# Kernel tuning notes

Measured on AMD Instinct MI355X. Metric: run time of the kernel, lower is better.

The kernel has to match this reference:

```python
import jax, jax.numpy as jnp
import numpy as np

N, E, FEAT, H, C = 50000, 800000, 256, 256, 64
THETA = 0.5


def _l2norm(x, eps=1e-12):
    n = jnp.sqrt(jnp.sum(x * x, axis=-1, keepdims=True))
    return x / jnp.maximum(n, eps)


def _gcn_conv(x, row, col, W, b):
    # x: [N, Fin]; row/col: [E+N] (self loops already appended); all edge weights are 1
    n = x.shape[0]
    h = x @ W                                                   # [N, Fout]
    ones = jnp.ones(row.shape, dtype=h.dtype)
    deg = jax.ops.segment_sum(ones, row, num_segments=n)        # in-degree over rows
    deg_safe = jnp.where(deg > 0, deg, 1.0)
    dinv = jnp.where(deg > 0, jax.lax.rsqrt(deg_safe), 0.0)
    norm = dinv[row] * dinv[col]                                # [E+N]
    msg = norm[:, None] * h[col]                                # gather + weight
    out = jax.ops.segment_sum(msg, row, num_segments=n)         # scatter-add
    return out + b


def setup_inputs() -> dict:
    key = jax.random.key(0)
    ks = jax.random.split(key, 10)
    edge_index = jax.random.randint(ks[0], (2, E), 0, N, dtype=jnp.int32)
    neg_edge_index = jax.random.randint(ks[1], (2, E), 0, N, dtype=jnp.int32)
    features = jax.random.normal(ks[2], (N, FEAT), dtype=jnp.float32)
    label_smoothing = jax.random.uniform(ks[3], (E,), dtype=jnp.float32)
    W1 = jax.random.normal(ks[4], (FEAT, H), dtype=jnp.float32) / np.sqrt(FEAT)
    b1 = jnp.zeros((H,), dtype=jnp.float32)
    W2 = jax.random.normal(ks[5], (H, H), dtype=jnp.float32) / np.sqrt(H)
    b2 = jnp.zeros((H,), dtype=jnp.float32)
    Wy = jax.random.normal(ks[6], (H, C), dtype=jnp.float32) / np.sqrt(H)
    by = jnp.zeros((C,), dtype=jnp.float32)
    return {"edge_index": edge_index, "features": features,
            "label_smoothing": label_smoothing, "neg_edge_index": neg_edge_index,
            "W1": W1, "b1": b1, "W2": W2, "b2": b2, "Wy": Wy, "by": by}


def reference(edge_index, features, label_smoothing, neg_edge_index,
              W1, b1, W2, b2, Wy, by):
    n = features.shape[0]
    self_idx = jnp.arange(n, dtype=edge_index.dtype)
    row = jnp.concatenate([edge_index[0], self_idx])
    col = jnp.concatenate([edge_index[1], self_idx])

    # GCN (dropout=0.0)
    x1 = jax.nn.relu(_gcn_conv(features, row, col, W1, b1))
    x2 = _gcn_conv(x1, row, col, W2, b2)
    rep = _l2norm(x2)
    rep = _l2norm(rep)  # second normalize in q_phi1.forward
    y = rep @ Wy + by

    # reconstruct_loss (i<j filtering done via static-shape masks)
    e0, e1 = edge_index[0], edge_index[1]
    n0, n1 = neg_edge_index[0], neg_edge_index[1]
    pos_mask = (e0 < e1).astype(rep.dtype)
    neg_mask = (n0 < n1).astype(rep.dtype)

    neg_w = jax.nn.relu(jnp.sum(rep[n0] * rep[n1], axis=1))
    pos_w = jax.nn.relu(jnp.sum(rep[e0] * rep[e1], axis=1))
    pos_fsim = jnp.sum(features[e0] * features[e1], axis=1)
    pos = pos_fsim * THETA + pos_w * (1.0 - THETA)

    n_pos = jnp.sum(pos_mask)
    n_neg = jnp.sum(neg_mask)
    neg_loss = jnp.sum(neg_mask * neg_w * neg_w)
    pos_loss = jnp.sum(pos_mask * (pos - label_smoothing) ** 2)
    rec_loss = (neg_loss + pos_loss) * n / (n_neg + n_pos)
    return rep, rec_loss, y
```

## Files before the change

### kernel.cpp

```cpp
#include <hip/hip_runtime.h>
#include <hip/hip_bf16.h>

#define FEAT 256
#define HDIM 256
#define CDIM 64
#define THETA 0.5f
#define APAD 264

typedef float floatx2 __attribute__((ext_vector_type(2)));
typedef __attribute__((ext_vector_type(8))) short bf16x8;
typedef __attribute__((ext_vector_type(4))) float f32x4;

__device__ __forceinline__ unsigned short f2bf(float f) {
    unsigned int u = __float_as_uint(f);
    u += 0x7fffu + ((u >> 16) & 1u);
    return (unsigned short)(u >> 16);
}
__device__ __forceinline__ unsigned char f2f8(float f) {
    int w = __builtin_amdgcn_cvt_pk_fp8_f32(f, f, 0, false);
    return (unsigned char)(w & 0xff);
}

__global__ __launch_bounds__(256) void prep(const int* __restrict__ e0, const int* __restrict__ e1,
                                            const int* __restrict__ n0, const int* __restrict__ n1,
                                            int* deg, int* __restrict__ blkP, int* __restrict__ blkN,
                                            const float* __restrict__ features, unsigned char* __restrict__ feat8,
                                            const float* __restrict__ W1, unsigned short* __restrict__ Wt1,
                                            const float* __restrict__ W2, unsigned short* __restrict__ Wt2,
                                            const float* __restrict__ Wy, unsigned short* __restrict__ WyT,
                                            int E, int n8, int ebk, int f8bk) {
    const int b = blockIdx.x;
    const int tid = threadIdx.x;
    if (b < ebk) {
        const int i = b * 256 + tid;
        const int lane = tid & 63;
        const int w = tid >> 6;
        bool vp = false, vn = false;
        if (i < E) {
            int a = e0[i], bb = e1[i];
            atomicAdd(&deg[a], 1);
            vp = a < bb;
            vn = n0[i] < n1[i];
        }
        unsigned long long mp = __ballot(vp);
        unsigned long long mn = __ballot(vn);
        __shared__ int s[8];
        if (lane == 0) {
            s[w] = __popcll(mp);
            s[4 + w] = __popcll(mn);
        }
        __syncthreads();
        if (tid == 0) blkP[b] = s[0] + s[1] + s[2] + s[3];
        if (tid == 1) blkN[b] = s[4] + s[5] + s[6] + s[7];
    } else if (b < ebk + f8bk) {
        int i = (b - ebk) * 256 + tid;
        if (i < n8) {
            float4 a = ((const float4*)features)[2 * i];
            float4 v = ((const float4*)features)[2 * i + 1];
            int w0 = __builtin_amdgcn_cvt_pk_fp8_f32(a.x, a.y, 0, false);
            w0 = __builtin_amdgcn_cvt_pk_fp8_f32(a.z, a.w, w0, true);
            int w1 = __builtin_amdgcn_cvt_pk_fp8_f32(v.x, v.y, 0, false);
            w1 = __builtin_amdgcn_cvt_pk_fp8_f32(v.z, v.w, w1, true);
            uint2 o;
            o.x = (unsigned int)w0;
            o.y = (unsigned int)w1;
            ((uint2*)feat8)[i] = o;
        }
    } else if (b < ebk + f8bk + 256) {
        int k = b - ebk - f8bk;
        Wt1[(size_t)tid * 256 + k] = f2bf(W1[(size_t)k * 256 + tid]);
    } else if (b < ebk + f8bk + 512) {
        int k = b - ebk - f8bk - 256;
        Wt2[(size_t)tid * 256 + k] = f2bf(W2[(size_t)k * 256 + tid]);
    } else {
        int b3 = b - ebk - f8bk - 512;
        int n = tid & 63;
        int k = b3 * 4 + (tid >> 6);
        WyT[(size_t)n * 256 + k] = f2bf(Wy[(size_t)k * 64 + n]);
    }
}

__global__ __launch_bounds__(256) void scan1_dinv(const int* __restrict__ deg,
                                                  int* __restrict__ rowptr,
                                                  int* __restrict__ blkS,
                                                  float* __restrict__ dinv, int N) {
    __shared__ int sh[256];
    const int tid = threadIdx.x;
    const int i = blockIdx.x * 256 + tid;
    int v = (i < N) ? deg[i] : 0;
    if (i < N) dinv[i] = rsqrtf((float)(v + 1));
    sh[tid] = v;
    __syncthreads();
#pragma unroll
    for (int off = 1; off < 256; off <<= 1) {
        int t = (tid >= off) ? sh[tid - off] : 0;
        __syncthreads();
        sh[tid] += t;
        __syncthreads();
    }
    if (i < N) rowptr[i] = sh[tid] - v;
    if (tid == 255) blkS[blockIdx.x] = sh[255];
}

__global__ __launch_bounds__(256) void scan2x(int* __restrict__ blkS, int nbn,
                                              int* __restrict__ blkP, int* __restrict__ blkN,
                                              int* __restrict__ cnt, int nb) {
    const int tid = threadIdx.x;
    if (blockIdx.x == 0) {
        __shared__ int part[256];
        const int chunk = (nbn + 255) / 256;
        const int s = tid * chunk;
        const int e = min(s + chunk, nbn);
        int sum = 0;
        for (int i = s; i < e; ++i) sum += blkS[i];
        part[tid] = sum;
        __syncthreads();
#pragma unroll
        for (int off = 1; off < 256; off <<= 1) {
            int t = (tid >= off) ? part[tid - off] : 0;
            __syncthreads();
            part[tid] += t;
            __syncthreads();
        }
        int run = part[tid] - sum;
        for (int i = s; i < e; ++i) {
            int v = blkS[i];
            blkS[i] = run;
            run += v;
        }
    } else {
        __shared__ int partP[256], partN[256];
        const int chunk = (nb + 255) / 256;
        const int s = tid * chunk;
        const int e = min(s + chunk, nb);
        int sp = 0, sn = 0;
        for (int i = s; i < e; ++i) { sp += blkP[i]; sn += blkN[i]; }
        partP[tid] = sp;
        partN[tid] = sn;
        __syncthreads();
#pragma unroll
        for (int off = 1; off < 256; off <<= 1) {
            int tp = (tid >= off) ? partP[tid - off] : 0;
            int tn = (tid >= off) ? partN[tid - off] : 0;
            __syncthreads();
            partP[tid] += tp;
            partN[tid] += tn;
            __syncthreads();
        }
        int runP = partP[tid] - sp;
        int runN = partN[tid] - sn;
        for (int i = s; i < e; ++i) {
            int vp = blkP[i], vn = blkN[i];
            blkP[i] = runP;
            blkN[i] = runN;
            runP += vp;
            runN += vn;
        }
        if (tid == 255) { cnt[0] = runP; cnt[1] = runN; }
    }
}

__global__ __launch_bounds__(256) void scan3_scatter(int* __restrict__ rowptr, int* __restrict__ cursor,
                                                     const int* __restrict__ blkS, int N, int E, int nbn,
                                                     const int* __restrict__ e0, const int* __restrict__ e1,
                                                     const int* __restrict__ n0, const int* __restrict__ n1,
                                                     const float* __restrict__ ls,
                                                     const int* __restrict__ blkP, const int* __restrict__ blkN,
                                                     int2* __restrict__ posAB, float* __restrict__ posLS,
                                                     int2* __restrict__ negCD) {
    const int b = blockIdx.x;
    const int tid = threadIdx.x;
    if (b < nbn) {
        const int i = b * 256 + tid;
        if (i < N) {
            int v = rowptr[i] + blkS[b];
            rowptr[i] = v;
            cursor[i] = v;
        }
        if (i == 0) rowptr[N] = E;
        return;
    }
    const int eb = b - nbn;
    const int i = eb * 256 + tid;
    const int lane = tid & 63;
    const int w = tid >> 6;
    const unsigned long long below = (lane == 0) ? 0ull : ((1ull << lane) - 1ull);
    int a = 0, bb = 0, c = 0, d = 0;
    float lsv = 0.f;
    bool vp = false, vn = false;
    if (i < E) {
        a = e0[i]; bb = e1[i];
        c = n0[i]; d = n1[i];
        vp = a < bb;
        vn = c < d;
        if (vp) lsv = ls[i];
    }
    unsigned long long mp = __ballot(vp);
    unsigned long long mn = __ballot(vn);
    __shared__ int sP[4], sN[4];
    if (lane == 0) {
        sP[w] = __popcll(mp);
        sN[w] = __popcll(mn);
    }
    __syncthreads();
    int baseP = blkP[eb];
    int baseN = blkN[eb];
    for (int q = 0; q < 4; ++q) {
        if (q < w) { baseP += sP[q]; baseN += sN[q]; }
    }
    if (vp) {
        int ofs = __popcll(mp & below);
        posAB[baseP + ofs] = make_int2(a, bb);
        posLS[baseP + ofs] = lsv;
    }
    if (vn) {
        int ofs = __popcll(mn & below);
        negCD[baseN + ofs] = make_int2(c, d);
    }
}

__global__ __launch_bounds__(256) void bucket_edges(const int* __restrict__ e0,
                                                    const int* __restrict__ e1,
                                                    int* cursor, int* __restrict__ colIdx, int E) {
    int i = blockIdx.x * 256 + threadIdx.x;
    if (i < E) {
        int r = e0[i];
        int pos = atomicAdd(&cursor[r], 1);
        colIdx[pos] = e1[i];
    }
}

__device__ __forceinline__ void gemm_core_f8out(const unsigned short* Al,
                                                const unsigned short* __restrict__ Wt,
                                                unsigned char* __restrict__ out,
                                                int m0, int wv, int lane, int M) {
    f32x4 acc[4][4] = {};
    const int r16 = lane & 15;
    const int kg8 = (lane >> 4) * 8;
    const unsigned short* wbase = Wt + ((size_t)(wv * 64 + r16)) * 256 + kg8;
    const unsigned short* abase = Al + r16 * APAD + kg8;

#pragma unroll
    for (int k0 = 0; k0 < 256; k0 += 32) {
        bf16x8 af[4], bfr[4];
#pragma unroll
        for (int mi = 0; mi < 4; ++mi)
            af[mi] = *(const bf16x8*)&abase[mi * 16 * APAD + k0];
#pragma unroll
        for (int ni = 0; ni < 4; ++ni)
            bfr[ni] = *(const bf16x8*)&wbase[ni * 16 * 256 + k0];
#pragma unroll
        for (int mi = 0; mi < 4; ++mi)
#pragma unroll
            for (int ni = 0; ni < 4; ++ni)
                acc[mi][ni] = __builtin_amdgcn_mfma_f32_16x16x32_bf16(af[mi], bfr[ni], acc[mi][ni], 0, 0, 0);
    }

#pragma unroll
    for (int mi = 0; mi < 4; ++mi) {
        int rbase = m0 + mi * 16 + ((lane >> 4) << 2);
#pragma unroll
        for (int ni = 0; ni < 4; ++ni) {
            int col = (wv << 6) + (ni << 4) + (lane & 15);
#pragma unroll
            for (int j = 0; j < 4; ++j) {
                int row = rbase + j;
                if (row < M) out[(size_t)row * 256 + col] = f2f8(acc[mi][ni][j]);
            }
        }
    }
}

__global__ __launch_bounds__(256) void gemm_mfma_f32A(const float* __restrict__ A,
                                                      const unsigned short* __restrict__ Wt,
                                                      unsigned char* __restrict__ out, int M) {
    __shared__ unsigned short Al[64 * APAD];
    const int tid = threadIdx.x;
    const int m0 = blockIdx.x * 64;
#pragma unroll
    for (int i = 0; i < 8; ++i) {
        int u = i * 256 + tid;
        int r = u >> 5;
        int c8 = (u & 31) * 8;
        int row = m0 + r;
        float4 v0, v1;
        if (row < M) {
            v0 = *(const float4*)&A[(size_t)row * 256 + c8];
            v1 = *(const float4*)&A[(size_t)row * 256 + c8 + 4];
        } else {
            v0 = make_float4(0.f, 0.f, 0.f, 0.f);
            v1 = v0;
        }
        uint4 o;
        o.x = (unsigned int)f2bf(v0.x) | ((unsigned int)f2bf(v0.y) << 16);
        o.y = (unsigned int)f2bf(v0.z) | ((unsigned int)f2bf(v0.w) << 16);
        o.z = (unsigned int)f2bf(v1.x) | ((unsigned int)f2bf(v1.y) << 16);
        o.w = (unsigned int)f2bf(v1.z) | ((unsigned int)f2bf(v1.w) << 16);
        *(uint4*)&Al[r * APAD + c8] = o;
    }
    __syncthreads();
    gemm_core_f8out(Al, Wt, out, m0, tid >> 6, tid & 63, M);
}

__global__ __launch_bounds__(256) void gemm_mfma_b16A(const unsigned short* __restrict__ A,
                                                      const unsigned short* __restrict__ Wt,
                                                      unsigned char* __restrict__ out, int M) {
    __shared__ unsigned short Al[64 * APAD];
    const int tid = threadIdx.x;
    const int m0 = blockIdx.x * 64;
#pragma unroll
    for (int i = 0; i < 8; ++i) {
        int u = i * 256 + tid;
        int r = u >> 5;
        int c8 = (u & 31) * 8;
        int row = m0 + r;
        uint4 o = make_uint4(0, 0, 0, 0);
        if (row < M) o = *(const uint4*)&A[(size_t)row * 256 + c8];
        *(uint4*)&Al[r * APAD + c8] = o;
    }
    __syncthreads();
    gemm_core_f8out(Al, Wt, out, m0, tid >> 6, tid & 63, M);
}

__global__ __launch_bounds__(256) void gemm_wy_f8A(const unsigned char* __restrict__ rep8,
                                                   const unsigned short* __restrict__ WyT,
                                                   const float* __restrict__ bias,
                                                   float* __restrict__ out, int M) {
    __shared__ unsigned short Al[64 * APAD];
    const int tid = threadIdx.x;
    const int m0 = blockIdx.x * 64;
    const int wv = tid >> 6;
    const int lane = tid & 63;

#pragma unroll
    for (int i = 0; i < 4; ++i) {
        int u = i * 256 + tid;
        int r = u >> 4;
        int c16 = (u & 15) * 16;
        int row = m0 + r;
        uint4 v = make_uint4(0, 0, 0, 0);
        if (row < M) v = *(const uint4*)&rep8[(size_t)row * 256 + c16];
        unsigned int ws[4] = {v.x, v.y, v.z, v.w};
        unsigned int ow[8];
#pragma unroll
        for (int q = 0; q < 4; ++q) {
            floatx2 lo = __builtin_amdgcn_cvt_pk_f32_fp8((int)ws[q], false);
            floatx2 hi = __builtin_amdgcn_cvt_pk_f32_fp8((int)ws[q], true);
            ow[2 * q] = (unsigned int)f2bf(lo.x) | ((unsigned int)f2bf(lo.y) << 16);
            ow[2 * q + 1] = (unsigned int)f2bf(hi.x) | ((unsigned int)f2bf(hi.y) << 16);
        }
        *(uint4*)&Al[r * APAD + c16] = make_uint4(ow[0], ow[1], ow[2], ow[3]);
        *(uint4*)&Al[r * APAD + c16 + 8] = make_uint4(ow[4], ow[5], ow[6], ow[7]);
    }
    __syncthreads();

    f32x4 acc[4] = {};
    const int r16 = lane & 15;
    const int kg8 = (lane >> 4) * 8;
    const unsigned short* wbase = WyT + ((size_t)(wv * 16 + r16)) * 256 + kg8;
    const unsigned short* abase = Al + r16 * APAD + kg8;

#pragma unroll
    for (int k0 = 0; k0 < 256; k0 += 32) {
        bf16x8 bfr = *(const bf16x8*)&wbase[k0];
#pragma unroll
        for (int mi = 0; mi < 4; ++mi) {
            bf16x8 af = *(const bf16x8*)&abase[mi * 16 * APAD + k0];
            acc[mi] = __builtin_amdgcn_mfma_f32_16x16x32_bf16(af, bfr, acc[mi], 0, 0, 0);
        }
    }

    int col = (wv << 4) + (lane & 15);
    float bv = bias[col];
#pragma unroll
    for (int mi = 0; mi < 4; ++mi) {
        int rbase = m0 + mi * 16 + ((lane >> 4) << 2);
#pragma unroll
        for (int j = 0; j < 4; ++j) {
            int row = rbase + j;
            if (row < M) out[(size_t)row * 64 + col] = acc[mi][j] + bv;
        }
    }
}

template <int DO_NORM>
__global__ __launch_bounds__(256) void spmm_gather_f8(const int* __restrict__ rowptr,
                                                      const int* __restrict__ colIdx,
                                                      const unsigned char* __restrict__ h8,
                                                      const float* __restrict__ dinv,
                                                      const float* __restrict__ bias,
                                                      unsigned short* __restrict__ out_b16,
                                                      float* __restrict__ rep,
                                                      unsigned char* __restrict__ rep8,
                                                      int N) {
    int row = (blockIdx.x * 256 + threadIdx.x) >> 5;
    int l = threadIdx.x & 31;
    if (row >= N) return;
    int beg = rowptr[row];
    int end = rowptr[row + 1];
    float a0 = 0.f, a1 = 0.f, a2 = 0.f, a3 = 0.f, a4 = 0.f, a5 = 0.f, a6 = 0.f, a7 = 0.f;
    int j = beg;
    for (; j + 3 < end; j += 4) {
        int cc[4];
#pragma unroll
        for (int q = 0; q < 4; ++q) cc[q] = colIdx[j + q];
        float ww[4];
#pragma unroll
        for (int q = 0; q < 4; ++q) ww[q] = dinv[cc[q]];
        uint2 uu[4];
#pragma unroll
        for (int q = 0; q < 4; ++q) uu[q] = *(const uint2*)&h8[(size_t)cc[q] * 256 + l * 8];
#pragma unroll
        for (int q = 0; q < 4; ++q) {
            floatx2 p0 = __builtin_amdgcn_cvt_pk_f32_fp8((int)uu[q].x, false);
            floatx2 p1 = __builtin_amdgcn_cvt_pk_f32_fp8((int)uu[q].x, true);
            floatx2 p2 = __builtin_amdgcn_cvt_pk_f32_fp8((int)uu[q].y, false);
            floatx2 p3 = __builtin_amdgcn_cvt_pk_f32_fp8((int)uu[q].y, true);
            a0 = fmaf(ww[q], p0.x, a0); a1 = fmaf(ww[q], p0.y, a1);
            a2 = fmaf(ww[q], p1.x, a2); a3 = fmaf(ww[q], p1.y, a3);
            a4 = fmaf(ww[q], p2.x, a4); a5 = fmaf(ww[q], p2.y, a5);
            a6 = fmaf(ww[q], p3.x, a6); a7 = fmaf(ww[q], p3.y, a7);
        }
    }
    for (; j < end; ++j) {
        int c = colIdx[j];
        float w = dinv[c];
        uint2 u = *(const uint2*)&h8[(size_t)c * 256 + l * 8];
        floatx2 p0 = __builtin_amdgcn_cvt_pk_f32_fp8((int)u.x, false);
        floatx2 p1 = __builtin_amdgcn_cvt_pk_f32_fp8((int)u.x, true);
        floatx2 p2 = __builtin_amdgcn_cvt_pk_f32_fp8((int)u.y, false);
        floatx2 p3 = __builtin_amdgcn_cvt_pk_f32_fp8((int)u.y, true);
        a0 = fmaf(w, p0.x, a0); a1 = fmaf(w, p0.y, a1);
        a2 = fmaf(w, p1.x, a2); a3 = fmaf(w, p1.y, a3);
        a4 = fmaf(w, p2.x, a4); a5 = fmaf(w, p2.y, a5);
        a6 = fmaf(w, p3.x, a6); a7 = fmaf(w, p3.y, a7);
    }
    float di = dinv[row];
    float s = di * di;
    uint2 us = *(const uint2*)&h8[(size_t)row * 256 + l * 8];
    floatx2 s0 = __builtin_amdgcn_cvt_pk_f32_fp8((int)us.x, false);
    floatx2 s1 = __builtin_amdgcn_cvt_pk_f32_fp8((int)us.x, true);
    floatx2 s2 = __builtin_amdgcn_cvt_pk_f32_fp8((int)us.y, false);
    floatx2 s3 = __builtin_amdgcn_cvt_pk_f32_fp8((int)us.y, true);
    float4 bv0 = *(const float4*)&bias[l * 8];
    float4 bv1 = *(const float4*)&bias[l * 8 + 4];
    float r0 = fmaf(di, a0, fmaf(s, s0.x, bv0.x));
    float r1 = fmaf(di, a1, fmaf(s, s0.y, bv0.y));
    float r2 = fmaf(di, a2, fmaf(s, s1.x, bv0.z));
    float r3 = fmaf(di, a3, fmaf(s, s1.y, bv0.w));
    float r4 = fmaf(di, a4, fmaf(s, s2.x, bv1.x));
    float r5 = fmaf(di, a5, fmaf(s, s2.y, bv1.y));
    float r6 = fmaf(di, a6, fmaf(s, s3.x, bv1.z));
    float r7 = fmaf(di, a7, fmaf(s, s3.y, bv1.w));
    if (DO_NORM == 0) {
        r0 = fmaxf(r0, 0.f); r1 = fmaxf(r1, 0.f); r2 = fmaxf(r2, 0.f); r3 = fmaxf(r3, 0.f);
        r4 = fmaxf(r4, 0.f); r5 = fmaxf(r5, 0.f); r6 = fmaxf(r6, 0.f); r7 = fmaxf(r7, 0.f);
        uint4 o;
        o.x = (unsigned int)f2bf(r0) | ((unsigned int)f2bf(r1) << 16);
        o.y = (unsigned int)f2bf(r2) | ((unsigned int)f2bf(r3) << 16);
        o.z = (unsigned int)f2bf(r4) | ((unsigned int)f2bf(r5) << 16);
        o.w = (unsigned int)f2bf(r6) | ((unsigned int)f2bf(r7) << 16);
        *(uint4*)&out_b16[(size_t)row * 256 + l * 8] = o;
    } else {
        float ss = r0 * r0 + r1 * r1 + r2 * r2 + r3 * r3 + r4 * r4 + r5 * r5 + r6 * r6 + r7 * r7;
#pragma unroll
        for (int o = 1; o < 32; o <<= 1) ss += __shfl_xor(ss, o);
        float inv = 1.0f / fmaxf(sqrtf(ss), 1e-12f);
        r0 *= inv; r1 *= inv; r2 *= inv; r3 *= inv;
        r4 *= inv; r5 *= inv; r6 *= inv; r7 *= inv;
        float ss2 = r0 * r0 + r1 * r1 + r2 * r2 + r3 * r3 + r4 * r4 + r5 * r5 + r6 * r6 + r7 * r7;
#pragma unroll
        for (int o = 1; o < 32; o <<= 1) ss2 += __shfl_xor(ss2, o);
        float inv2 = 1.0f / fmaxf(sqrtf(ss2), 1e-12f);
        r0 *= inv2; r1 *= inv2; r2 *= inv2; r3 *= inv2;
        r4 *= inv2; r5 *= inv2; r6 *= inv2; r7 *= inv2;
        *(float4*)&rep[(size_t)row * 256 + l * 8] = make_float4(r0, r1, r2, r3);
        *(float4*)&rep[(size_t)row * 256 + l * 8 + 4] = make_float4(r4, r5, r6, r7);
        int w0 = __builtin_amdgcn_cvt_pk_fp8_f32(r0, r1, 0, false);
        w0 = __builtin_amdgcn_cvt_pk_fp8_f32(r2, r3, w0, true);
        int w1 = __builtin_amdgcn_cvt_pk_fp8_f32(r4, r5, 0, false);
        w1 = __builtin_amdgcn_cvt_pk_fp8_f32(r6, r7, w1, true);
        uint2 o;
        o.x = (unsigned int)w0;
        o.y = (unsigned int)w1;
        *(uint2*)&rep8[(size_t)row * 256 + l * 8] = o;
    }
}

__device__ __forceinline__ float dot16fp8(uint4 x, uint4 y) {
    float s = 0.f;
    const unsigned int xs[4] = {x.x, x.y, x.z, x.w};
    const unsigned int ys[4] = {y.x, y.y, y.z, y.w};
#pragma unroll
    for (int i = 0; i < 4; ++i) {
        floatx2 xl = __builtin_amdgcn_cvt_pk_f32_fp8((int)xs[i], false);
        floatx2 xh = __builtin_amdgcn_cvt_pk_f32_fp8((int)xs[i], true);
        floatx2 yl = __builtin_amdgcn_cvt_pk_f32_fp8((int)ys[i], false);
        floatx2 yh = __builtin_amdgcn_cvt_pk_f32_fp8((int)ys[i], true);
        s += xl.x * yl.x + xl.y * yl.y + xh.x * yh.x + xh.y * yh.y;
    }
    return s;
}

__global__ __launch_bounds__(256) void loss_all(const int2* __restrict__ posAB,
                                                const float* __restrict__ posLS,
                                                const int2* __restrict__ negCD,
                                                const int* __restrict__ cnt,
                                                const unsigned char* __restrict__ rep8,
                                                const unsigned char* __restrict__ feat8,
                                                float* accum) {
    const int tid = threadIdx.x;
    const int l8 = tid & 7;
    const int grp = (blockIdx.x * 256 + tid) >> 3;
    const int ngrp = gridDim.x * 32;
    const int P = cnt[0];
    const int T = P + cnt[1];
    float ap = 0.f, an = 0.f;
    for (int g = grp; g < T; g += ngrp) {
        if (g < P) {
            int2 ab = posAB[g];
            const uint4* pra = (const uint4*)&rep8[(size_t)ab.x * 256 + l8 * 32];
            const uint4* prb = (const uint4*)&rep8[(size_t)ab.y * 256 + l8 * 32];
            const uint4* pfa = (const uint4*)&feat8[(size_t)ab.x * 256 + l8 * 32];
            const uint4* pfb = (const uint4*)&feat8[(size_t)ab.y * 256 + l8 * 32];
            uint4 ra0 = pra[0], ra1 = pra[1];
            uint4 rb0 = prb[0], rb1 = prb[1];
            uint4 fa0 = pfa[0], fa1 = pfa[1];
            uint4 fb0 = pfb[0], fb1 = pfb[1];
            float dp = dot16fp8(ra0, rb0) + dot16fp8(ra1, rb1);
            float df = dot16fp8(fa0, fb0) + dot16fp8(fa1, fb1);
#pragma unroll
            for (int o = 1; o < 8; o <<= 1) {
                dp += __shfl_xor(dp, o);
                df += __shfl_xor(df, o);
            }
            if (l8 == 0) {
                float pw = fmaxf(dp, 0.f);
                float pos = THETA * df + (1.0f - THETA) * pw;
                float t = pos - posLS[g];
                ap += t * t;
            }
        } else {
            int2 cd = negCD[g - P];
            const uint4* prc = (const uint4*)&rep8[(size_t)cd.x * 256 + l8 * 32];
            const uint4* prd = (const uint4*)&rep8[(size_t)cd.y * 256 + l8 * 32];
            uint4 rc0 = prc[0], rc1 = prc[1];
            uint4 rd0 = prd[0], rd1 = prd[1];
            float dn = dot16fp8(rc0, rd0) + dot16fp8(rc1, rd1);
#pragma unroll
            for (int o = 1; o < 8; o <<= 1) dn += __shfl_xor(dn, o);
            if (l8 == 0) {
                float nwt = fmaxf(dn, 0.f);
                an += nwt * nwt;
            }
        }
    }
#pragma unroll
    for (int o = 1; o < 64; o <<= 1) {
        ap += __shfl_xor(ap, o);
        an += __shfl_xor(an, o);
    }
    __shared__ float s[4][2];
    if ((tid & 63) == 0) {
        s[tid >> 6][0] = ap;
        s[tid >> 6][1] = an;
    }
    __syncthreads();
    if (tid == 0) {
        unsafeAtomicAdd(&accum[0], s[0][0] + s[1][0] + s[2][0] + s[3][0]);
        unsafeAtomicAdd(&accum[1], s[0][1] + s[1][1] + s[2][1] + s[3][1]);
    }
}

__global__ void loss_final(const float* __restrict__ accum, const int* __restrict__ cnt,
                           float* __restrict__ out, int N) {
    out[0] = (accum[0] + accum[1]) * (float)N / (float)(cnt[0] + cnt[1]);
}

extern "C" void kernel_launch(void* const* d_in, const int* in_sizes, int n_in,
                              void* d_out, int out_size, void* d_ws, size_t ws_size,
                              hipStream_t stream) {
    const int* edge = (const int*)d_in[0];
    const float* features = (const float*)d_in[1];
    const float* ls = (const float*)d_in[2];
    const int* nedge = (const int*)d_in[3];
    const float* W1 = (const float*)d_in[4];
    const float* b1 = (const float*)d_in[5];
    const float* W2 = (const float*)d_in[6];
    const float* b2 = (const float*)d_in[7];
    const float* Wy = (const float*)d_in[8];
    const float* by = (const float*)d_in[9];

    const int E = in_sizes[0] / 2;
    const int N = in_sizes[1] / FEAT;
    const int* e0 = edge;
    const int* e1 = edge + E;
    const int* n0 = nedge;
    const int* n1 = nedge + E;

    float* rep = (float*)d_out;
    float* rec = rep + (size_t)N * 256;
    float* y = rec + 1;

    char* base = (char*)d_ws;
    size_t off = 0;
    auto carve = [&](size_t bytes) -> void* {
        void* p = base + off;
        off += (bytes + 1023) & ~(size_t)1023;
        return p;
    };
    int* deg = (int*)carve((size_t)N * 4);
    float* dinv = (float*)carve((size_t)N * 4);
    float* accum = (float*)carve(16);
    int* cnt = (int*)carve(16);
    int* rowptr = (int*)carve((size_t)(N + 1) * 4);
    int* cursor = (int*)carve((size_t)N * 4);
    int* colIdx = (int*)carve((size_t)E * 4);
    unsigned char* h8 = (unsigned char*)carve((size_t)N * 256);
    unsigned short* x1B = (unsigned short*)carve((size_t)N * 256 * 2);
    unsigned char* feat8 = (unsigned char*)carve((size_t)N * 256);
    unsigned char* rep8 = (unsigned char*)carve((size_t)N * 256);
    unsigned short* Wt1 = (unsigned short*)carve(256 * 256 * 2);
    unsigned short* Wt2 = (unsigned short*)carve(256 * 256 * 2);
    unsigned short* WyT = (unsigned short*)carve(64 * 256 * 2);
    int2* posAB = (int2*)carve((size_t)E * 8);
    float* posLS = (float*)carve((size_t)E * 4);
    int2* negCD = (int2*)carve((size_t)E * 8);
    const int ebk = (E + 255) / 256;
    int* blkP = (int*)carve((size_t)ebk * 4);
    int* blkN = (int*)carve((size_t)ebk * 4);
    const int nbn = (N + 255) / 256;
    int* blkS = (int*)carve((size_t)nbn * 4);

    const int n8 = N * 256 / 8;
    const int f8bk = (n8 + 255) / 256;
    const int gblk = (N + 63) / 64;
    const int wblk32 = (N + 7) / 8;

    hipMemsetAsync(deg, 0, (size_t)N * 4, stream);
    hipMemsetAsync(accum, 0, 16, stream);

    prep<<<ebk + f8bk + 512 + 64, 256, 0, stream>>>(e0, e1, n0, n1, deg, blkP, blkN,
                                                    features, feat8, W1, Wt1, W2, Wt2, Wy, WyT,
                                                    E, n8, ebk, f8bk);

    scan1_dinv<<<nbn, 256, 0, stream>>>(deg, rowptr, blkS, dinv, N);
    scan2x<<<2, 256, 0, stream>>>(blkS, nbn, blkP, blkN, cnt, ebk);
    scan3_scatter<<<nbn + ebk, 256, 0, stream>>>(rowptr, cursor, blkS, N, E, nbn,
                                                 e0, e1, n0, n1, ls, blkP, blkN, posAB, posLS, negCD);
    bucket_edges<<<ebk, 256, 0, stream>>>(e0, e1, cursor, colIdx, E);

    gemm_mfma_f32A<<<gblk, 256, 0, stream>>>(features, Wt1, h8, N);
    spmm_gather_f8<0><<<wblk32, 256, 0, stream>>>(rowptr, colIdx, h8, dinv, b1, x1B, nullptr, nullptr, N);

    gemm_mfma_b16A<<<gblk, 256, 0, stream>>>(x1B, Wt2, h8, N);
    spmm_gather_f8<1><<<wblk32, 256, 0, stream>>>(rowptr, colIdx, h8, dinv, b2, nullptr, rep, rep8, N);

    gemm_wy_f8A<<<gblk, 256, 0, stream>>>(rep8, WyT, by, y, N);

    loss_all<<<2048, 256, 0, stream>>>(posAB, posLS, negCD, cnt, rep8, feat8, accum);
    loss_final<<<1, 1, 0, stream>>>(accum, cnt, rec, N);
}
```

Before: 370.8 us.

## Prescale GEMM output by dinv, fuse feature fp8 cast, interleave rep/feat rows

The GEMM epilogues now multiply each output row by dinv[row], so the SpMM gather no longer loads a per-neighbor dinv and just sums fp8 values. The fp8 cast of features moves out of the prep kernel into the first GEMM's A-load, removing a separate pass over the features array. rep8 and feat8 are interleaved into one 512-byte-per-node buffer so the positive-edge loss fetches both from adjacent memory. Scaling before fp8 quantization slightly changes rounding, and the wider row stride halves locality for negative-edge and Wy reads.

```diff
diff --git a/kernel.cpp b/kernel.cpp
--- a/kernel.cpp
+++ b/kernel.cpp
@@ -24,11 +24,10 @@
 __global__ __launch_bounds__(256) void prep(const int* __restrict__ e0, const int* __restrict__ e1,
                                             const int* __restrict__ n0, const int* __restrict__ n1,
                                             int* deg, int* __restrict__ blkP, int* __restrict__ blkN,
-                                            const float* __restrict__ features, unsigned char* __restrict__ feat8,
                                             const float* __restrict__ W1, unsigned short* __restrict__ Wt1,
                                             const float* __restrict__ W2, unsigned short* __restrict__ Wt2,
                                             const float* __restrict__ Wy, unsigned short* __restrict__ WyT,
-                                            int E, int n8, int ebk, int f8bk) {
+                                            int E, int ebk) {
     const int b = blockIdx.x;
     const int tid = threadIdx.x;
     if (b < ebk) {
@@ -52,28 +51,14 @@
         __syncthreads();
         if (tid == 0) blkP[b] = s[0] + s[1] + s[2] + s[3];
         if (tid == 1) blkN[b] = s[4] + s[5] + s[6] + s[7];
-    } else if (b < ebk + f8bk) {
-        int i = (b - ebk) * 256 + tid;
-        if (i < n8) {
-            float4 a = ((const float4*)features)[2 * i];
-            float4 v = ((const float4*)features)[2 * i + 1];
-            int w0 = __builtin_amdgcn_cvt_pk_fp8_f32(a.x, a.y, 0, false);
-            w0 = __builtin_amdgcn_cvt_pk_fp8_f32(a.z, a.w, w0, true);
-            int w1 = __builtin_amdgcn_cvt_pk_fp8_f32(v.x, v.y, 0, false);
-            w1 = __builtin_amdgcn_cvt_pk_fp8_f32(v.z, v.w, w1, true);
-            uint2 o;
-            o.x = (unsigned int)w0;
-            o.y = (unsigned int)w1;
-            ((uint2*)feat8)[i] = o;
-        }
-    } else if (b < ebk + f8bk + 256) {
-        int k = b - ebk - f8bk;
+    } else if (b < ebk + 256) {
+        int k = b - ebk;
         Wt1[(size_t)tid * 256 + k] = f2bf(W1[(size_t)k * 256 + tid]);
-    } else if (b < ebk + f8bk + 512) {
-        int k = b - ebk - f8bk - 256;
+    } else if (b < ebk + 512) {
+        int k = b - ebk - 256;
         Wt2[(size_t)tid * 256 + k] = f2bf(W2[(size_t)k * 256 + tid]);
     } else {
-        int b3 = b - ebk - f8bk - 512;
+        int b3 = b - ebk - 512;
         int n = tid & 63;
         int k = b3 * 4 + (tid >> 6);
         WyT[(size_t)n * 256 + k] = f2bf(Wy[(size_t)k * 64 + n]);
@@ -231,6 +216,7 @@
 }
 
 __device__ __forceinline__ void gemm_core_f8out(const unsigned short* Al,
+                                                const float* sd,
                                                 const unsigned short* __restrict__ Wt,
                                                 unsigned char* __restrict__ out,
                                                 int m0, int wv, int lane, int M) {
@@ -265,18 +251,22 @@
 #pragma unroll
             for (int j = 0; j < 4; ++j) {
                 int row = rbase + j;
-                if (row < M) out[(size_t)row * 256 + col] = f2f8(acc[mi][ni][j]);
+                if (row < M) out[(size_t)row * 256 + col] = f2f8(sd[row - m0] * acc[mi][ni][j]);
             }
         }
     }
 }
 
 __global__ __launch_bounds__(256) void gemm_mfma_f32A(const float* __restrict__ A,
+                                                      const float* __restrict__ dinv,
                                                       const unsigned short* __restrict__ Wt,
-                                                      unsigned char* __restrict__ out, int M) {
+                                                      unsigned char* __restrict__ out,
+                                                      unsigned char* __restrict__ repfeat8, int M) {
     __shared__ unsigned short Al[64 * APAD];
+    __shared__ float sd[64];
     const int tid = threadIdx.x;
     const int m0 = blockIdx.x * 64;
+    if (tid < 64) sd[tid] = (m0 + tid < M) ? dinv[m0 + tid] : 0.f;
 #pragma unroll
     for (int i = 0; i < 8; ++i) {
         int u = i * 256 + tid;
@@ -297,17 +287,30 @@
         o.z = (unsigned int)f2bf(v1.x) | ((unsigned int)f2bf(v1.y) << 16);
         o.w = (unsigned int)f2bf(v1.z) | ((unsigned int)f2bf(v1.w) << 16);
         *(uint4*)&Al[r * APAD + c8] = o;
+        if (row < M) {
+            int w0 = __builtin_amdgcn_cvt_pk_fp8_f32(v0.x, v0.y, 0, false);
+            w0 = __builtin_amdgcn_cvt_pk_fp8_f32(v0.z, v0.w, w0, true);
+            int w1 = __builtin_amdgcn_cvt_pk_fp8_f32(v1.x, v1.y, 0, false);
+            w1 = __builtin_amdgcn_cvt_pk_fp8_f32(v1.z, v1.w, w1, true);
+            uint2 f;
+            f.x = (unsigned int)w0;
+            f.y = (unsigned int)w1;
+            *(uint2*)&repfeat8[(size_t)row * 512 + 256 + c8] = f;
+        }
     }
     __syncthreads();
-    gemm_core_f8out(Al, Wt, out, m0, tid >> 6, tid & 63, M);
+    gemm_core_f8out(Al, sd, Wt, out, m0, tid >> 6, tid & 63, M);
 }
 
 __global__ __launch_bounds__(256) void gemm_mfma_b16A(const unsigned short* __restrict__ A,
+                                                      const float* __restrict__ dinv,
                                                       const unsigned short* __restrict__ Wt,
                                                       unsigned char* __restrict__ out, int M) {
     __shared__ unsigned short Al[64 * APAD];
+    __shared__ float sd[64];
     const int tid = threadIdx.x;
     const int m0 = blockIdx.x * 64;
+    if (tid < 64) sd[tid] = (m0 + tid < M) ? dinv[m0 + tid] : 0.f;
 #pragma unroll
     for (int i = 0; i < 8; ++i) {
         int u = i * 256 + tid;
@@ -319,10 +322,10 @@
         *(uint4*)&Al[r * APAD + c8] = o;
     }
     __syncthreads();
-    gemm_core_f8out(Al, Wt, out, m0, tid >> 6, tid & 63, M);
-}
-
-__global__ __launch_bounds__(256) void gemm_wy_f8A(const unsigned char* __restrict__ rep8,
+    gemm_core_f8out(Al, sd, Wt, out, m0, tid >> 6, tid & 63, M);
+}
+
+__global__ __launch_bounds__(256) void gemm_wy_f8A(const unsigned char* __restrict__ repfeat8,
                                                    const unsigned short* __restrict__ WyT,
                                                    const float* __restrict__ bias,
                                                    float* __restrict__ out, int M) {
@@ -339,7 +342,7 @@
         int c16 = (u & 15) * 16;
         int row = m0 + r;
         uint4 v = make_uint4(0, 0, 0, 0);
-        if (row < M) v = *(const uint4*)&rep8[(size_t)row * 256 + c16];
+        if (row < M) v = *(const uint4*)&repfeat8[(size_t)row * 512 + c16];
         unsigned int ws[4] = {v.x, v.y, v.z, v.w};
         unsigned int ow[8];
 #pragma unroll
@@ -386,12 +389,12 @@
 template <int DO_NORM>
 __global__ __launch_bounds__(256) void spmm_gather_f8(const int* __restrict__ rowptr,
                                                       const int* __restrict__ colIdx,
-                                                      const unsigned char* __restrict__ h8,
+                                                      const unsigned char* __restrict__ g8,
                                                       const float* __restrict__ dinv,
                                                       const float* __restrict__ bias,
                                                       unsigned short* __restrict__ out_b16,
                                                       float* __restrict__ rep,
-                                                      unsigned char* __restrict__ rep8,
+                                                      unsigned char* __restrict__ repfeat8,
                                                       int N) {
     int row = (blockIdx.x * 256 + threadIdx.x) >> 5;
     int l = threadIdx.x & 31;
@@ -404,54 +407,45 @@
         int cc[4];
 #pragma unroll
         for (int q = 0; q < 4; ++q) cc[q] = colIdx[j + q];
-        float ww[4];
-#pragma unroll
-        for (int q = 0; q < 4; ++q) ww[q] = dinv[cc[q]];
         uint2 uu[4];
 #pragma unroll
-        for (int q = 0; q < 4; ++q) uu[q] = *(const uint2*)&h8[(size_t)cc[q] * 256 + l * 8];
+        for (int q = 0; q < 4; ++q) uu[q] = *(const uint2*)&g8[(size_t)cc[q] * 256 + l * 8];
 #pragma unroll
         for (int q = 0; q < 4; ++q) {
             floatx2 p0 = __builtin_amdgcn_cvt_pk_f32_fp8((int)uu[q].x, false);
             floatx2 p1 = __builtin_amdgcn_cvt_pk_f32_fp8((int)uu[q].x, true);
             floatx2 p2 = __builtin_amdgcn_cvt_pk_f32_fp8((int)uu[q].y, false);
             floatx2 p3 = __builtin_amdgcn_cvt_pk_f32_fp8((int)uu[q].y, true);
-            a0 = fmaf(ww[q], p0.x, a0); a1 = fmaf(ww[q], p0.y, a1);
-            a2 = fmaf(ww[q], p1.x, a2); a3 = fmaf(ww[q], p1.y, a3);
-            a4 = fmaf(ww[q], p2.x, a4); a5 = fmaf(ww[q], p2.y, a5);
-            a6 = fmaf(ww[q], p3.x, a6); a7 = fmaf(ww[q], p3.y, a7);
+            a0 += p0.x; a1 += p0.y; a2 += p1.x; a3 += p1.y;
+            a4 += p2.x; a5 += p2.y; a6 += p3.x; a7 += p3.y;
         }
     }
     for (; j < end; ++j) {
         int c = colIdx[j];
-        float w = dinv[c];
-        uint2 u = *(const uint2*)&h8[(size_t)c * 256 + l * 8];
+        uint2 u = *(const uint2*)&g8[(size_t)c * 256 + l * 8];
         floatx2 p0 = __builtin_amdgcn_cvt_pk_f32_fp8((int)u.x, false);
         floatx2 p1 = __builtin_amdgcn_cvt_pk_f32_fp8((int)u.x, true);
         floatx2 p2 = __builtin_amdgcn_cvt_pk_f32_fp8((int)u.y, false);
         floatx2 p3 = __builtin_amdgcn_cvt_pk_f32_fp8((int)u.y, true);
-        a0 = fmaf(w, p0.x, a0); a1 = fmaf(w, p0.y, a1);
-        a2 = fmaf(w, p1.x, a2); a3 = fmaf(w, p1.y, a3);
-        a4 = fmaf(w, p2.x, a4); a5 = fmaf(w, p2.y, a5);
-        a6 = fmaf(w, p3.x, a6); a7 = fmaf(w, p3.y, a7);
+        a0 += p0.x; a1 += p0.y; a2 += p1.x; a3 += p1.y;
+        a4 += p2.x; a5 += p2.y; a6 += p3.x; a7 += p3.y;
     }
     float di = dinv[row];
-    float s = di * di;
-    uint2 us = *(const uint2*)&h8[(size_t)row * 256 + l * 8];
+    uint2 us = *(const uint2*)&g8[(size_t)row * 256 + l * 8];
     floatx2 s0 = __builtin_amdgcn_cvt_pk_f32_fp8((int)us.x, false);
     floatx2 s1 = __builtin_amdgcn_cvt_pk_f32_fp8((int)us.x, true);
     floatx2 s2 = __builtin_amdgcn_cvt_pk_f32_fp8((int)us.y, false);
     floatx2 s3 = __builtin_amdgcn_cvt_pk_f32_fp8((int)us.y, true);
     float4 bv0 = *(const float4*)&bias[l * 8];
     float4 bv1 = *(const float4*)&bias[l * 8 + 4];
-    float r0 = fmaf(di, a0, fmaf(s, s0.x, bv0.x));
-    float r1 = fmaf(di, a1, fmaf(s, s0.y, bv0.y));
-    float r2 = fmaf(di, a2, fmaf(s, s1.x, bv0.z));
-    float r3 = fmaf(di, a3, fmaf(s, s1.y, bv0.w));
-    float r4 = fmaf(di, a4, fmaf(s, s2.x, bv1.x));
-    float r5 = fmaf(di, a5, fmaf(s, s2.y, bv1.y));
-    float r6 = fmaf(di, a6, fmaf(s, s3.x, bv1.z));
-    float r7 = fmaf(di, a7, fmaf(s, s3.y, bv1.w));
+    float r0 = fmaf(di, a0 + s0.x, bv0.x);
+    float r1 = fmaf(di, a1 + s0.y, bv0.y);
+    float r2 = fmaf(di, a2 + s1.x, bv0.z);
+    float r3 = fmaf(di, a3 + s1.y, bv0.w);
+    float r4 = fmaf(di, a4 + s2.x, bv1.x);
+    float r5 = fmaf(di, a5 + s2.y, bv1.y);
+    float r6 = fmaf(di, a6 + s3.x, bv1.z);
+    float r7 = fmaf(di, a7 + s3.y, bv1.w);
     if (DO_NORM == 0) {
         r0 = fmaxf(r0, 0.f); r1 = fmaxf(r1, 0.f); r2 = fmaxf(r2, 0.f); r3 = fmaxf(r3, 0.f);
         r4 = fmaxf(r4, 0.f); r5 = fmaxf(r5, 0.f); r6 = fmaxf(r6, 0.f); r7 = fmaxf(r7, 0.f);
@@ -483,7 +477,7 @@
         uint2 o;
         o.x = (unsigned int)w0;
         o.y = (unsigned int)w1;
-        *(uint2*)&rep8[(size_t)row * 256 + l * 8] = o;
+        *(uint2*)&repfeat8[(size_t)row * 512 + l * 8] = o;
     }
 }
 
@@ -506,8 +500,7 @@
                                                 const float* __restrict__ posLS,
                                                 const int2* __restrict__ negCD,
                                                 const int* __restrict__ cnt,
-                                                const unsigned char* __restrict__ rep8,
-                                                const unsigned char* __restrict__ feat8,
+                                                const unsigned char* __restrict__ repfeat8,
                                                 float* accum) {
     const int tid = threadIdx.x;
     const int l8 = tid & 7;
@@ -519,14 +512,16 @@
     for (int g = grp; g < T; g += ngrp) {
         if (g < P) {
             int2 ab = posAB[g];
-            const uint4* pra = (const uint4*)&rep8[(size_t)ab.x * 256 + l8 * 32];
-            const uint4* prb = (const uint4*)&rep8[(size_t)ab.y * 256 + l8 * 32];
-            const uint4* pfa = (const uint4*)&feat8[(size_t)ab.x * 256 + l8 * 32];
-            const uint4* pfb = (const uint4*)&feat8[(size_t)ab.y * 256 + l8 * 32];
-            uint4 ra0 = pra[0], ra1 = pra[1];
-            uint4 rb0 = prb[0], rb1 = prb[1];
-            uint4 fa0 = pfa[0], fa1 = pfa[1];
-            uint4 fb0 = pfb[0], fb1 = pfb[1];
+            const unsigned char* pa = &repfeat8[(size_t)ab.x * 512 + l8 * 32];
+            const unsigned char* pb = &repfeat8[(size_t)ab.y * 512 + l8 * 32];
+            uint4 ra0 = *(const uint4*)pa;
+            uint4 ra1 = *(const uint4*)(pa + 16);
+            uint4 fa0 = *(const uint4*)(pa + 256);
+            uint4 fa1 = *(const uint4*)(pa + 272);
+            uint4 rb0 = *(const uint4*)pb;
+            uint4 rb1 = *(const uint4*)(pb + 16);
+            uint4 fb0 = *(const uint4*)(pb + 256);
+            uint4 fb1 = *(const uint4*)(pb + 272);
             float dp = dot16fp8(ra0, rb0) + dot16fp8(ra1, rb1);
             float df = dot16fp8(fa0, fb0) + dot16fp8(fa1, fb1);
 #pragma unroll
@@ -542,10 +537,12 @@
             }
         } else {
             int2 cd = negCD[g - P];
-            const uint4* prc = (const uint4*)&rep8[(size_t)cd.x * 256 + l8 * 32];
-            const uint4* prd = (const uint4*)&rep8[(size_t)cd.y * 256 + l8 * 32];
-            uint4 rc0 = prc[0], rc1 = prc[1];
-            uint4 rd0 = prd[0], rd1 = prd[1];
+            const unsigned char* pc = &repfeat8[(size_t)cd.x * 512 + l8 * 32];
+            const unsigned char* pd = &repfeat8[(size_t)cd.y * 512 + l8 * 32];
+            uint4 rc0 = *(const uint4*)pc;
+            uint4 rc1 = *(const uint4*)(pc + 16);
+            uint4 rd0 = *(const uint4*)pd;
+            uint4 rd1 = *(const uint4*)(pd + 16);
             float dn = dot16fp8(rc0, rd0) + dot16fp8(rc1, rd1);
 #pragma unroll
             for (int o = 1; o < 8; o <<= 1) dn += __shfl_xor(dn, o);
@@ -616,10 +613,9 @@
     int* rowptr = (int*)carve((size_t)(N + 1) * 4);
     int* cursor = (int*)carve((size_t)N * 4);
     int* colIdx = (int*)carve((size_t)E * 4);
-    unsigned char* h8 = (unsigned char*)carve((size_t)N * 256);
+    unsigned char* g8 = (unsigned char*)carve((size_t)N * 256);
     unsigned short* x1B = (unsigned short*)carve((size_t)N * 256 * 2);
-    unsigned char* feat8 = (unsigned char*)carve((size_t)N * 256);
-    unsigned char* rep8 = (unsigned char*)carve((size_t)N * 256);
+    unsigned char* repfeat8 = (unsigned char*)carve((size_t)N * 512);
     unsigned short* Wt1 = (unsigned short*)carve(256 * 256 * 2);
     unsigned short* Wt2 = (unsigned short*)carve(256 * 256 * 2);
     unsigned short* WyT = (unsigned short*)carve(64 * 256 * 2);
@@ -632,17 +628,14 @@
     const int nbn = (N + 255) / 256;
     int* blkS = (int*)carve((size_t)nbn * 4);
 
-    const int n8 = N * 256 / 8;
-    const int f8bk = (n8 + 255) / 256;
     const int gblk = (N + 63) / 64;
     const int wblk32 = (N + 7) / 8;
 
     hipMemsetAsync(deg, 0, (size_t)N * 4, stream);
     hipMemsetAsync(accum, 0, 16, stream);
 
-    prep<<<ebk + f8bk + 512 + 64, 256, 0, stream>>>(e0, e1, n0, n1, deg, blkP, blkN,
-                                                    features, feat8, W1, Wt1, W2, Wt2, Wy, WyT,
-                                                    E, n8, ebk, f8bk);
+    prep<<<ebk + 512 + 64, 256, 0, stream>>>(e0, e1, n0, n1, deg, blkP, blkN,
+                                             W1, Wt1, W2, Wt2, Wy, WyT, E, ebk);
 
     scan1_dinv<<<nbn, 256, 0, stream>>>(deg, rowptr, blkS, dinv, N);
     scan2x<<<2, 256, 0, stream>>>(blkS, nbn, blkP, blkN, cnt, ebk);
@@ -650,14 +643,14 @@
                                                  e0, e1, n0, n1, ls, blkP, blkN, posAB, posLS, negCD);
     bucket_edges<<<ebk, 256, 0, stream>>>(e0, e1, cursor, colIdx, E);
 
-    gemm_mfma_f32A<<<gblk, 256, 0, stream>>>(features, Wt1, h8, N);
-    spmm_gather_f8<0><<<wblk32, 256, 0, stream>>>(rowptr, colIdx, h8, dinv, b1, x1B, nullptr, nullptr, N);
-
-    gemm_mfma_b16A<<<gblk, 256, 0, stream>>>(x1B, Wt2, h8, N);
-    spmm_gather_f8<1><<<wblk32, 256, 0, stream>>>(rowptr, colIdx, h8, dinv, b2, nullptr, rep, rep8, N);
-
-    gemm_wy_f8A<<<gblk, 256, 0, stream>>>(rep8, WyT, by, y, N);
-
-    loss_all<<<2048, 256, 0, stream>>>(posAB, posLS, negCD, cnt, rep8, feat8, accum);
+    gemm_mfma_f32A<<<gblk, 256, 0, stream>>>(features, dinv, Wt1, g8, repfeat8, N);
+    spmm_gather_f8<0><<<wblk32, 256, 0, stream>>>(rowptr, colIdx, g8, dinv, b1, x1B, nullptr, nullptr, N);
+
+    gemm_mfma_b16A<<<gblk, 256, 0, stream>>>(x1B, dinv, Wt2, g8, N);
+    spmm_gather_f8<1><<<wblk32, 256, 0, stream>>>(rowptr, colIdx, g8, dinv, b2, nullptr, rep, repfeat8, N);
+
+    gemm_wy_f8A<<<gblk, 256, 0, stream>>>(repfeat8, WyT, by, y, N);
+
+    loss_all<<<2048, 256, 0, stream>>>(posAB, posLS, negCD, cnt, repfeat8, accum);
     loss_final<<<1, 1, 0, stream>>>(accum, cnt, rec, N);
 }
```

Result: no change. 372.1 us (+0.3%).
